# Optimization experiments

Measured on AMD Instinct MI355X. Metric: run time of the kernel, lower is better.

## Reference

```python
import jax, jax.numpy as jnp
import numpy as np

NUM_CELLS = 8
NEIGHBORHOOD = 2.0
H_DIM = 64
ATT_DIM = 32
EMBED_DIM = 4
NUM_PED = 2048
NUM_POINTS = 8192


def setup_inputs() -> dict:
    key = jax.random.key(0)
    ks = jax.random.split(key, 12)
    s = 0.05
    return {
        "scene_info": jax.random.normal(ks[0], (NUM_POINTS, 2), jnp.float32) * 2.0,
        "curr_end_pos": jax.random.normal(ks[1], (NUM_PED, 2), jnp.float32) * 2.0,
        "curr_disp_pos": jax.random.normal(ks[2], (NUM_PED, 2), jnp.float32) * 0.1,
        "curr_hidden_1": jax.random.normal(ks[3], (NUM_PED, H_DIM), jnp.float32),
        "W_enc": jax.random.normal(ks[4], (1, ATT_DIM), jnp.float32) * s,
        "b_enc": jnp.zeros((ATT_DIM,), jnp.float32),
        "W_dec": jax.random.normal(ks[5], (H_DIM, ATT_DIM), jnp.float32) * s,
        "b_dec": jnp.zeros((ATT_DIM,), jnp.float32),
        "W_full": jax.random.normal(ks[6], (ATT_DIM, 1), jnp.float32) * s,
        "b_full": jnp.zeros((1,), jnp.float32),
        "W_fbeta": jax.random.normal(ks[7], (H_DIM, 1), jnp.float32) * s,
        "b_fbeta": jnp.zeros((1,), jnp.float32),
        "W_emb": jax.random.normal(ks[8], (4, EMBED_DIM), jnp.float32) * s,
        "b_emb": jnp.zeros((EMBED_DIM,), jnp.float32),
        "W_ih": jax.random.normal(ks[9], (EMBED_DIM + 1, 4 * H_DIM), jnp.float32) * s,
        "b_ih": jnp.zeros((4 * H_DIM,), jnp.float32),
        "W_hh": jax.random.normal(ks[10], (H_DIM, 4 * H_DIM), jnp.float32) * s,
        "b_hh": jnp.zeros((4 * H_DIM,), jnp.float32),
        "num_ped": NUM_PED,
    }


def _occupancy_grid(scene_info, curr_end_pos, num_ped):
    """Per-pedestrian occupancy grid via bounds-check + scatter_add. -> [N, G*G, 1]"""
    G = NUM_CELLS
    total = G * G
    half = NEIGHBORHOOD / 2.0
    px, py = curr_end_pos[:, 0], curr_end_pos[:, 1]          # [N]
    tlx, tly = px - half, py + half                          # top-left
    brx, bry = px + half, py - half                          # bottom-right
    sx, sy = scene_info[:, 0], scene_info[:, 1]              # [P]
    # [N, P] grid cell ids (same math as torch: floor in float, +1, +per-ped offset)
    cell_x = jnp.floor((sx[None, :] - tlx[:, None]) / NEIGHBORHOOD * G)
    cell_y = jnp.floor((tly[:, None] - sy[None, :]) / NEIGHBORHOOD * G)
    grid_pos = cell_x + cell_y * G + 1.0
    grid_pos = grid_pos + (jnp.arange(num_ped, dtype=jnp.float32) * total)[:, None]
    # torch: x_bound/y_bound are OR-ed 'outside' predicates; outside -> slot 0 (dropped)
    outside = ((sx[None, :] >= brx[:, None]) | (sx[None, :] <= tlx[:, None]) |
               (sy[None, :] >= tly[:, None]) | (sy[None, :] <= bry[:, None]))
    idx = jnp.where(outside, 0.0, grid_pos).astype(jnp.int32).reshape(-1)
    counts = jax.ops.segment_sum(
        jnp.ones(idx.shape[0], jnp.float32), idx, num_segments=num_ped * total + 1)
    return counts[1:].reshape(num_ped, total, 1)


def _attention_decoder(encoder_out, h, embed_info,
                       W_enc, b_enc, W_dec, b_dec, W_full, b_full,
                       W_fbeta, b_fbeta, W_emb, b_emb, W_ih, b_ih, W_hh, b_hh):
    # Show-Attend-Tell style additive attention over grid cells
    att1 = encoder_out @ W_enc + b_enc                       # [N, total, ATT]
    att2 = h @ W_dec + b_dec                                 # [N, ATT]
    att = (jax.nn.relu(att1 + att2[:, None, :]) @ W_full + b_full)[..., 0]  # [N, total]
    alpha = jax.nn.softmax(att, axis=1)
    awe = jnp.sum(encoder_out * alpha[..., None], axis=1)    # [N, 1]
    gate = jax.nn.sigmoid(h @ W_fbeta + b_fbeta)             # [N, 1]
    awe = gate * awe
    emb = embed_info @ W_emb + b_emb                         # [N, EMBED_DIM]
    x = jnp.concatenate([emb, awe], axis=1)                  # [N, EMBED_DIM+1]
    # LSTMCell step with (h0=h, c0=0), torch gate order i,f,g,o
    gates = x @ W_ih + b_ih + h @ W_hh + b_hh                # [N, 4H]
    i, f, g, o = jnp.split(gates, 4, axis=1)
    c = jax.nn.sigmoid(i) * jnp.tanh(g)
    return jax.nn.sigmoid(o) * jnp.tanh(c)


def reference(scene_info, curr_end_pos, curr_disp_pos, curr_hidden_1,
              W_enc, b_enc, W_dec, b_dec, W_full, b_full, W_fbeta, b_fbeta,
              W_emb, b_emb, W_ih, b_ih, W_hh, b_hh, num_ped):
    h = curr_hidden_1.reshape(-1, H_DIM)
    embed_info = jnp.concatenate([curr_end_pos, curr_disp_pos], axis=1)  # [N, 4]
    encoder_out = _occupancy_grid(scene_info, curr_end_pos, num_ped)
    curr_pool_h = _attention_decoder(encoder_out, h, embed_info,
                                     W_enc, b_enc, W_dec, b_dec, W_full, b_full,
                                     W_fbeta, b_fbeta, W_emb, b_emb,
                                     W_ih, b_ih, W_hh, b_hh)
    return curr_pool_h
```

## Files before the change

kernel.cpp:

```cpp
#include <hip/hip_runtime.h>


constexpr int CELLS = 64;
constexpr int HD    = 64;
constexpr int AD    = 32;
constexpr int PPB   = 2;
constexpr int BLK   = 256;

__device__ __forceinline__ float fsig(float x) {
    return __builtin_amdgcn_rcpf(1.f + __expf(-x));
}
__device__ __forceinline__ float ftanh(float x) {
    float e = __expf(2.f * x);
    return 1.f - 2.f * __builtin_amdgcn_rcpf(e + 1.f);
}

__global__ __launch_bounds__(BLK, 4) void fused_ssfe_kernel(
    const float* __restrict__ scene,
    const float* __restrict__ end_pos,
    const float* __restrict__ disp_pos,
    const float* __restrict__ h_in,
    const float* __restrict__ W_enc,
    const float* __restrict__ b_enc,
    const float* __restrict__ W_dec,
    const float* __restrict__ b_dec,
    const float* __restrict__ W_full,
    const float* __restrict__ b_full,
    const float* __restrict__ W_fbeta,
    const float* __restrict__ b_fbeta,
    const float* __restrict__ W_emb,
    const float* __restrict__ b_emb,
    const float* __restrict__ W_ih,
    const float* __restrict__ b_ih,
    const float* __restrict__ W_hh,
    const float* __restrict__ b_hh,
    float* __restrict__ out,
    int nped, int npts)
{
    __shared__ unsigned hist[PPB][CELLS];
    __shared__ float    h_s[PPB][HD];
    __shared__ float    att2_s[PPB][AD];
    __shared__ float    part[PPB][3][HD];

    const int tid  = threadIdx.x;
    const int ped0 = blockIdx.x * PPB;
    const int wave = tid >> 6;
    const int lane = tid & 63;
    const int p    = wave & 1;
    const int half = wave >> 1;
    const int ped  = ped0 + p;

    if (tid < PPB * CELLS) ((unsigned*)hist)[tid] = 0u;
    if (tid < PPB * HD) {
        int pp = tid >> 6, k = tid & 63;
        int pd = ped0 + pp;
        h_s[pp][k] = (pd < nped) ? h_in[pd * HD + k] : 0.f;
    }

    float px0, py0, px1, py1;
    px0 = end_pos[ped0 * 2 + 0]; py0 = end_pos[ped0 * 2 + 1];
    if (ped0 + 1 < nped) { px1 = end_pos[ped0 * 2 + 2]; py1 = end_pos[ped0 * 2 + 3]; }
    else                 { px1 = 1e30f;                 py1 = 1e30f; }
    const float tlx0 = px0 - 1.0f, tly0 = py0 + 1.0f, brx0 = px0 + 1.0f, bry0 = py0 - 1.0f;
    const float tlx1 = px1 - 1.0f, tly1 = py1 + 1.0f, brx1 = px1 + 1.0f, bry1 = py1 - 1.0f;
    __syncthreads();

    {
        const float4* sc4 = reinterpret_cast<const float4*>(scene);
        const int n4 = npts >> 1;
        #pragma unroll 4
        for (int i = tid; i < n4; i += BLK) {
            float4 s = sc4[i];
            {
                bool o = (s.x >= brx0) | (s.x <= tlx0) | (s.y >= tly0) | (s.y <= bry0);
                if (!o) {
                    int c = (int)(floorf((s.x - tlx0) * 4.f) + floorf((tly0 - s.y) * 4.f) * 8.f);
                    atomicAdd(&hist[0][c], 1u);
                }
            }
            {
                bool o = (s.x >= brx1) | (s.x <= tlx1) | (s.y >= tly1) | (s.y <= bry1);
                if (!o) {
                    int c = (int)(floorf((s.x - tlx1) * 4.f) + floorf((tly1 - s.y) * 4.f) * 8.f);
                    atomicAdd(&hist[1][c], 1u);
                }
            }
            {
                bool o = (s.z >= brx0) | (s.z <= tlx0) | (s.w >= tly0) | (s.w <= bry0);
                if (!o) {
                    int c = (int)(floorf((s.z - tlx0) * 4.f) + floorf((tly0 - s.w) * 4.f) * 8.f);
                    atomicAdd(&hist[0][c], 1u);
                }
            }
            {
                bool o = (s.z >= brx1) | (s.z <= tlx1) | (s.w >= tly1) | (s.w <= bry1);
                if (!o) {
                    int c = (int)(floorf((s.z - tlx1) * 4.f) + floorf((tly1 - s.w) * 4.f) * 8.f);
                    atomicAdd(&hist[1][c], 1u);
                }
            }
        }
    }
    __syncthreads();

    float acc_i, acc_g, acc_o;

    if (half == 1) {
        if (ped < nped) {
            acc_i = 0.f; acc_g = 0.f; acc_o = 0.f;
            #pragma unroll 8
            for (int k = 32; k < 64; ++k) {
                float hk = h_s[p][k];
                acc_i = fmaf(hk, W_hh[k * 256 + lane],       acc_i);
                acc_g = fmaf(hk, W_hh[k * 256 + 128 + lane], acc_g);
                acc_o = fmaf(hk, W_hh[k * 256 + 192 + lane], acc_o);
            }
            part[p][0][lane] = acc_i;
            part[p][1][lane] = acc_g;
            part[p][2][lane] = acc_o;
        }
    } else if (ped < nped) {
        {
            const int col   = lane & 31;
            const int kbase = (lane >> 5) * 32;
            float a = 0.f;
            #pragma unroll 8
            for (int k = 0; k < 32; ++k) {
                int kk = kbase + k;
                a = fmaf(h_s[p][kk], W_dec[kk * AD + col], a);
            }
            a += __shfl_xor(a, 32, 64);
            if (lane < AD) att2_s[p][lane] = a + b_dec[lane] + b_enc[lane];
        }
        float cnt = (float)hist[p][lane];
        float att = b_full[0];
        #pragma unroll 8
        for (int j = 0; j < AD; ++j) {
            float s = fmaf(cnt, W_enc[j], att2_s[p][j]);
            att = fmaf(fmaxf(s, 0.f), W_full[j], att);
        }
        float m = att;
        #pragma unroll
        for (int off = 32; off; off >>= 1) m = fmaxf(m, __shfl_xor(m, off, 64));
        float e = __expf(att - m);
        float ssum = e;
        #pragma unroll
        for (int off = 32; off; off >>= 1) ssum += __shfl_xor(ssum, off, 64);
        float awe = cnt * e * __builtin_amdgcn_rcpf(ssum);
        #pragma unroll
        for (int off = 32; off; off >>= 1) awe += __shfl_xor(awe, off, 64);

        float gp = h_s[p][lane] * W_fbeta[lane];
        #pragma unroll
        for (int off = 32; off; off >>= 1) gp += __shfl_xor(gp, off, 64);
        float gate = fsig(gp + b_fbeta[0]);
        float aweg = gate * awe;

        float dx = disp_pos[ped * 2], dy = disp_pos[ped * 2 + 1];
        float ex = (p == 0) ? px0 : px1;
        float ey = (p == 0) ? py0 : py1;
        float x0 = ex * W_emb[0]  + ey * W_emb[4]  + dx * W_emb[8]  + dy * W_emb[12] + b_emb[0];
        float x1 = ex * W_emb[1]  + ey * W_emb[5]  + dx * W_emb[9]  + dy * W_emb[13] + b_emb[1];
        float x2 = ex * W_emb[2]  + ey * W_emb[6]  + dx * W_emb[10] + dy * W_emb[14] + b_emb[2];
        float x3 = ex * W_emb[3]  + ey * W_emb[7]  + dx * W_emb[11] + dy * W_emb[15] + b_emb[3];

        acc_i = b_ih[lane]       + b_hh[lane];
        acc_g = b_ih[128 + lane] + b_hh[128 + lane];
        acc_o = b_ih[192 + lane] + b_hh[192 + lane];
        acc_i = fmaf(x0, W_ih[0 * 256 + lane], acc_i);
        acc_g = fmaf(x0, W_ih[0 * 256 + 128 + lane], acc_g);
        acc_o = fmaf(x0, W_ih[0 * 256 + 192 + lane], acc_o);
        acc_i = fmaf(x1, W_ih[1 * 256 + lane], acc_i);
        acc_g = fmaf(x1, W_ih[1 * 256 + 128 + lane], acc_g);
        acc_o = fmaf(x1, W_ih[1 * 256 + 192 + lane], acc_o);
        acc_i = fmaf(x2, W_ih[2 * 256 + lane], acc_i);
        acc_g = fmaf(x2, W_ih[2 * 256 + 128 + lane], acc_g);
        acc_o = fmaf(x2, W_ih[2 * 256 + 192 + lane], acc_o);
        acc_i = fmaf(x3, W_ih[3 * 256 + lane], acc_i);
        acc_g = fmaf(x3, W_ih[3 * 256 + 128 + lane], acc_g);
        acc_o = fmaf(x3, W_ih[3 * 256 + 192 + lane], acc_o);
        acc_i = fmaf(aweg, W_ih[4 * 256 + lane], acc_i);
        acc_g = fmaf(aweg, W_ih[4 * 256 + 128 + lane], acc_g);
        acc_o = fmaf(aweg, W_ih[4 * 256 + 192 + lane], acc_o);
        #pragma unroll 8
        for (int k = 0; k < 32; ++k) {
            float hk = h_s[p][k];
            acc_i = fmaf(hk, W_hh[k * 256 + lane],       acc_i);
            acc_g = fmaf(hk, W_hh[k * 256 + 128 + lane], acc_g);
            acc_o = fmaf(hk, W_hh[k * 256 + 192 + lane], acc_o);
        }
    }
    __syncthreads();

    if (half == 0 && ped < nped) {
        acc_i += part[p][0][lane];
        acc_g += part[p][1][lane];
        acc_o += part[p][2][lane];
        float cc = fsig(acc_i) * ftanh(acc_g);
        out[ped * HD + lane] = fsig(acc_o) * ftanh(cc);
    }
}

extern "C" void kernel_launch(void* const* d_in, const int* in_sizes, int n_in,
                              void* d_out, int out_size, void* d_ws, size_t ws_size,
                              hipStream_t stream)
{
    const float* scene   = (const float*)d_in[0];
    const float* end_pos = (const float*)d_in[1];
    const float* disp    = (const float*)d_in[2];
    const float* h_in    = (const float*)d_in[3];
    const float* W_enc   = (const float*)d_in[4];
    const float* b_enc   = (const float*)d_in[5];
    const float* W_dec   = (const float*)d_in[6];
    const float* b_dec   = (const float*)d_in[7];
    const float* W_full  = (const float*)d_in[8];
    const float* b_full  = (const float*)d_in[9];
    const float* W_fbeta = (const float*)d_in[10];
    const float* b_fbeta = (const float*)d_in[11];
    const float* W_emb   = (const float*)d_in[12];
    const float* b_emb   = (const float*)d_in[13];
    const float* W_ih    = (const float*)d_in[14];
    const float* b_ih    = (const float*)d_in[15];
    const float* W_hh    = (const float*)d_in[16];
    const float* b_hh    = (const float*)d_in[17];
    float* out = (float*)d_out;

    const int nped = in_sizes[1] / 2;
    const int npts = in_sizes[0] / 2;
    const int blocks = (nped + PPB - 1) / PPB;

    hipLaunchKernelGGL(fused_ssfe_kernel, dim3(blocks), dim3(BLK), 0, stream,
        scene, end_pos, disp, h_in, W_enc, b_enc, W_dec, b_dec, W_full, b_full,
        W_fbeta, b_fbeta, W_emb, b_emb, W_ih, b_ih, W_hh, b_hh, out, nped, npts);
}
```

Baseline: 17.44 us.

## Double block size, branchless histogram with dummy bins, split W_hh across three waves

The block grows to 512 threads, so each pedestrian pair gets four waves. The scene scan uses twice as many threads, and the hidden-to-hidden matvec is split across three waves so wave 0 only does the attention and input terms. The histogram binning becomes branchless: out-of-range points increment per-lane dummy bins instead of branching, so every point issues an atomic. The two softmax reductions are fused into one shuffle loop. The risks are more LDS atomics, lower block occupancy from the larger LDS and thread footprint, and the extra sync cost of bigger blocks.

```diff
diff --git a/kernel.cpp b/kernel.cpp
--- a/kernel.cpp
+++ b/kernel.cpp
@@ -1,11 +1,11 @@
 #include <hip/hip_runtime.h>
 
 
-constexpr int CELLS = 64;
 constexpr int HD    = 64;
 constexpr int AD    = 32;
 constexpr int PPB   = 2;
-constexpr int BLK   = 256;
+constexpr int BLK   = 512;
+constexpr int HROW  = 128;
 
 __device__ __forceinline__ float fsig(float x) {
     return __builtin_amdgcn_rcpf(1.f + __expf(-x));
@@ -15,7 +15,7 @@
     return 1.f - 2.f * __builtin_amdgcn_rcpf(e + 1.f);
 }
 
-__global__ __launch_bounds__(BLK, 4) void fused_ssfe_kernel(
+__global__ __launch_bounds__(BLK, 8) void fused_ssfe_kernel(
     const float* __restrict__ scene,
     const float* __restrict__ end_pos,
     const float* __restrict__ disp_pos,
@@ -37,20 +37,20 @@
     float* __restrict__ out,
     int nped, int npts)
 {
-    __shared__ unsigned hist[PPB][CELLS];
+    __shared__ unsigned hist[PPB][HROW];
     __shared__ float    h_s[PPB][HD];
     __shared__ float    att2_s[PPB][AD];
-    __shared__ float    part[PPB][3][HD];
+    __shared__ float    part[PPB][3][3][HD];
 
     const int tid  = threadIdx.x;
     const int ped0 = blockIdx.x * PPB;
     const int wave = tid >> 6;
     const int lane = tid & 63;
     const int p    = wave & 1;
-    const int half = wave >> 1;
+    const int r    = wave >> 1;
     const int ped  = ped0 + p;
 
-    if (tid < PPB * CELLS) ((unsigned*)hist)[tid] = 0u;
+    if (tid < PPB * HROW) ((unsigned*)hist)[tid] = 0u;
     if (tid < PPB * HD) {
         int pp = tid >> 6, k = tid & 63;
         int pd = ped0 + pp;
@@ -66,58 +66,46 @@
     __syncthreads();
 
     {
+        const int dummy = 64 + lane;
+        auto test = [&](float sx, float sy, int pp,
+                        float tlx, float tly, float brx, float bry) {
+            bool inside = (sx < brx) & (sx > tlx) & (sy < tly) & (sy > bry);
+            float cx = floorf((sx - tlx) * 4.0f);
+            float cy = floorf((tly - sy) * 4.0f);
+            int c = (int)fmaf(cy, 8.0f, cx);
+            int idx = inside ? c : dummy;
+            atomicAdd(&hist[pp][idx], 1u);
+        };
         const float4* sc4 = reinterpret_cast<const float4*>(scene);
         const int n4 = npts >> 1;
         #pragma unroll 4
         for (int i = tid; i < n4; i += BLK) {
             float4 s = sc4[i];
-            {
-                bool o = (s.x >= brx0) | (s.x <= tlx0) | (s.y >= tly0) | (s.y <= bry0);
-                if (!o) {
-                    int c = (int)(floorf((s.x - tlx0) * 4.f) + floorf((tly0 - s.y) * 4.f) * 8.f);
-                    atomicAdd(&hist[0][c], 1u);
-                }
-            }
-            {
-                bool o = (s.x >= brx1) | (s.x <= tlx1) | (s.y >= tly1) | (s.y <= bry1);
-                if (!o) {
-                    int c = (int)(floorf((s.x - tlx1) * 4.f) + floorf((tly1 - s.y) * 4.f) * 8.f);
-                    atomicAdd(&hist[1][c], 1u);
-                }
-            }
-            {
-                bool o = (s.z >= brx0) | (s.z <= tlx0) | (s.w >= tly0) | (s.w <= bry0);
-                if (!o) {
-                    int c = (int)(floorf((s.z - tlx0) * 4.f) + floorf((tly0 - s.w) * 4.f) * 8.f);
-                    atomicAdd(&hist[0][c], 1u);
-                }
-            }
-            {
-                bool o = (s.z >= brx1) | (s.z <= tlx1) | (s.w >= tly1) | (s.w <= bry1);
-                if (!o) {
-                    int c = (int)(floorf((s.z - tlx1) * 4.f) + floorf((tly1 - s.w) * 4.f) * 8.f);
-                    atomicAdd(&hist[1][c], 1u);
-                }
-            }
+            test(s.x, s.y, 0, tlx0, tly0, brx0, bry0);
+            test(s.x, s.y, 1, tlx1, tly1, brx1, bry1);
+            test(s.z, s.w, 0, tlx0, tly0, brx0, bry0);
+            test(s.z, s.w, 1, tlx1, tly1, brx1, bry1);
         }
     }
     __syncthreads();
 
-    float acc_i, acc_g, acc_o;
-
-    if (half == 1) {
+    float acc_i = 0.f, acc_g = 0.f, acc_o = 0.f;
+
+    if (r != 0) {
         if (ped < nped) {
-            acc_i = 0.f; acc_g = 0.f; acc_o = 0.f;
-            #pragma unroll 8
-            for (int k = 32; k < 64; ++k) {
+            int k0, k1;
+            if      (r == 1) { k0 = 0;  k1 = 22; }
+            else if (r == 2) { k0 = 22; k1 = 43; }
+            else             { k0 = 43; k1 = 64; }
+            for (int k = k0; k < k1; ++k) {
                 float hk = h_s[p][k];
                 acc_i = fmaf(hk, W_hh[k * 256 + lane],       acc_i);
                 acc_g = fmaf(hk, W_hh[k * 256 + 128 + lane], acc_g);
                 acc_o = fmaf(hk, W_hh[k * 256 + 192 + lane], acc_o);
             }
-            part[p][0][lane] = acc_i;
-            part[p][1][lane] = acc_g;
-            part[p][2][lane] = acc_o;
+            part[p][r - 1][0][lane] = acc_i;
+            part[p][r - 1][1][lane] = acc_g;
+            part[p][r - 1][2][lane] = acc_o;
         }
     } else if (ped < nped) {
         {
@@ -142,27 +130,27 @@
         float m = att;
         #pragma unroll
         for (int off = 32; off; off >>= 1) m = fmaxf(m, __shfl_xor(m, off, 64));
-        float e = __expf(att - m);
-        float ssum = e;
+        float e  = __expf(att - m);
+        float se = e, sa = cnt * e;
         #pragma unroll
-        for (int off = 32; off; off >>= 1) ssum += __shfl_xor(ssum, off, 64);
-        float awe = cnt * e * __builtin_amdgcn_rcpf(ssum);
-        #pragma unroll
-        for (int off = 32; off; off >>= 1) awe += __shfl_xor(awe, off, 64);
+        for (int off = 32; off; off >>= 1) {
+            se += __shfl_xor(se, off, 64);
+            sa += __shfl_xor(sa, off, 64);
+        }
+        float awe = sa * __builtin_amdgcn_rcpf(se);
 
         float gp = h_s[p][lane] * W_fbeta[lane];
         #pragma unroll
         for (int off = 32; off; off >>= 1) gp += __shfl_xor(gp, off, 64);
-        float gate = fsig(gp + b_fbeta[0]);
-        float aweg = gate * awe;
+        float aweg = fsig(gp + b_fbeta[0]) * awe;
 
         float dx = disp_pos[ped * 2], dy = disp_pos[ped * 2 + 1];
         float ex = (p == 0) ? px0 : px1;
         float ey = (p == 0) ? py0 : py1;
-        float x0 = ex * W_emb[0]  + ey * W_emb[4]  + dx * W_emb[8]  + dy * W_emb[12] + b_emb[0];
-        float x1 = ex * W_emb[1]  + ey * W_emb[5]  + dx * W_emb[9]  + dy * W_emb[13] + b_emb[1];
-        float x2 = ex * W_emb[2]  + ey * W_emb[6]  + dx * W_emb[10] + dy * W_emb[14] + b_emb[2];
-        float x3 = ex * W_emb[3]  + ey * W_emb[7]  + dx * W_emb[11] + dy * W_emb[15] + b_emb[3];
+        float x0 = ex * W_emb[0] + ey * W_emb[4] + dx * W_emb[8]  + dy * W_emb[12] + b_emb[0];
+        float x1 = ex * W_emb[1] + ey * W_emb[5] + dx * W_emb[9]  + dy * W_emb[13] + b_emb[1];
+        float x2 = ex * W_emb[2] + ey * W_emb[6] + dx * W_emb[10] + dy * W_emb[14] + b_emb[2];
+        float x3 = ex * W_emb[3] + ey * W_emb[7] + dx * W_emb[11] + dy * W_emb[15] + b_emb[3];
 
         acc_i = b_ih[lane]       + b_hh[lane];
         acc_g = b_ih[128 + lane] + b_hh[128 + lane];
@@ -182,20 +170,13 @@
         acc_i = fmaf(aweg, W_ih[4 * 256 + lane], acc_i);
         acc_g = fmaf(aweg, W_ih[4 * 256 + 128 + lane], acc_g);
         acc_o = fmaf(aweg, W_ih[4 * 256 + 192 + lane], acc_o);
-        #pragma unroll 8
-        for (int k = 0; k < 32; ++k) {
-            float hk = h_s[p][k];
-            acc_i = fmaf(hk, W_hh[k * 256 + lane],       acc_i);
-            acc_g = fmaf(hk, W_hh[k * 256 + 128 + lane], acc_g);
-            acc_o = fmaf(hk, W_hh[k * 256 + 192 + lane], acc_o);
-        }
     }
     __syncthreads();
 
-    if (half == 0 && ped < nped) {
-        acc_i += part[p][0][lane];
-        acc_g += part[p][1][lane];
-        acc_o += part[p][2][lane];
+    if (r == 0 && ped < nped) {
+        acc_i += part[p][0][0][lane] + part[p][1][0][lane] + part[p][2][0][lane];
+        acc_g += part[p][0][1][lane] + part[p][1][1][lane] + part[p][2][1][lane];
+        acc_o += part[p][0][2][lane] + part[p][1][2][lane] + part[p][2][2][lane];
         float cc = fsig(acc_i) * ftanh(acc_g);
         out[ped * HD + lane] = fsig(acc_o) * ftanh(cc);
     }
```

After: 16.74 us. 4.0% less time.
